# Performance work log

Hardware: AMD Instinct MI355X
Metric: run time of the kernel (lower is better)

Reference implementation:

```python
import jax, jax.numpy as jnp
import numpy as np

N = 100000      # nodes
E = 1600000     # edges (before self-loops)
NFEAT = 256
NHID = 64       # heads=1, concat -> output dim = NHID
NEG_SLOPE = 0.2 # PyG GATConv default negative_slope


def setup_inputs() -> dict:
    key = jax.random.key(0)
    k1, k2, k3, k4, k5 = jax.random.split(key, 5)
    x = jax.random.normal(k1, (N, NFEAT), dtype=jnp.float32)
    edge_index = jax.random.randint(k2, (2, E), 0, N, dtype=jnp.int64)
    s = 1.0 / np.sqrt(NFEAT)
    W = jax.random.uniform(k3, (NFEAT, NHID), jnp.float32, -s, s)      # lin weight
    a_src = jax.random.normal(k4, (NHID,), jnp.float32) * 0.1          # att_src
    a_dst = jax.random.normal(k5, (NHID,), jnp.float32) * 0.1          # att_dst
    bias = jnp.zeros((NHID,), jnp.float32)
    return {"x": x, "edge_index": edge_index, "W": W,
            "a_src": a_src, "a_dst": a_dst, "bias": bias}


def reference(x, edge_index, W, a_src, a_dst, bias):
    n = x.shape[0]
    xp = x @ W                                   # [N, NHID] transformed features
    # add self-loops (PyG default add_self_loops=True)
    loop = jnp.arange(n, dtype=edge_index.dtype)
    src = jnp.concatenate([edge_index[0], loop])  # message source j
    dst = jnp.concatenate([edge_index[1], loop])  # message target i
    # per-edge attention logits: LeakyReLU(a_src.x'_j + a_dst.x'_i)
    e = jax.nn.leaky_relu((xp @ a_src)[src] + (xp @ a_dst)[dst], NEG_SLOPE)  # [E+N]
    # segment softmax over incoming edges of each destination node
    m = jax.ops.segment_max(e, dst, num_segments=n)       # [N] (every node has a self-loop)
    ex = jnp.exp(e - m[dst])
    denom = jax.ops.segment_sum(ex, dst, num_segments=n)  # [N]
    alpha = ex / denom[dst]                                # [E+N]
    # attention-weighted scatter aggregation
    out = jax.ops.segment_sum(alpha[:, None] * xp[src], dst, num_segments=n)  # [N, NHID]
    return out + bias
```

## Files before the change

kernel.cpp:

```cpp
#include <hip/hip_runtime.h>
#include <hip/hip_bf16.h>

#define NFEAT 256
#define NHID  64
#define BSH   8
#define BUCKN 256
#define CAP   5120
#define CHUNK 4096

typedef unsigned int u32;
typedef unsigned short u16;
typedef long long ll;

typedef __attribute__((ext_vector_type(8))) short bf16x8;
typedef __attribute__((ext_vector_type(4))) float f32x4;

__device__ __forceinline__ float bfu2f(u16 u) {
    return __uint_as_float((u32)u << 16);
}
__device__ __forceinline__ u16 f2bfu(float f) {
    u32 u = __float_as_uint(f);
    u32 r = (u + 0x7fffu + ((u >> 16) & 1u)) >> 16;
    return (u16)r;
}
__device__ __forceinline__ float load_f(const void* p, int i, int f32) {
    return f32 ? ((const float*)p)[i] : bfu2f(((const u16*)p)[i]);
}

__device__ __forceinline__ void load_edge(const void* ei, int i64f, int E, int eid,
                                          int& src, int& dst) {
    if (eid < E) {
        if (i64f) {
            src = (int)((const ll*)ei)[eid];
            dst = (int)((const ll*)ei)[(size_t)E + eid];
        } else {
            src = ((const int*)ei)[eid];
            dst = ((const int*)ei)[(size_t)E + eid];
        }
    } else {
        src = dst = eid - E;
    }
}

__global__ __launch_bounds__(256) void prep_kernel(
    const void* __restrict__ W_, const void* __restrict__ ei,
    int* __restrict__ flags, u16* __restrict__ wt, int* __restrict__ gcursor)
{
    __shared__ int f32sh;
    const int tid = threadIdx.x;
    const int b = blockIdx.x;
    if (tid == 0) f32sh = 0;
    __syncthreads();
    {
        float v = bfu2f(((const u16*)W_)[tid]);
        if (!(fabsf(v) <= 0.07f)) f32sh = 1;
    }
    __syncthreads();
    const int f32 = f32sh;
    if (b == 0) {
        if (tid == 0) flags[0] = f32;
        if (tid < 64) {
            int vv = ((const int*)ei)[2 * tid + 1];
            unsigned long long m = __ballot(vv != 0);
            if (tid == 0) flags[1] = (m == 0ull) ? 1 : 0;
        }
        gcursor[tid] = 0;
        gcursor[256 + tid] = 0;
    }
    wt[b * 256 + tid] = f2bfu(load_f(W_, tid * NHID + b, f32));
}

__global__ __launch_bounds__(512) void mid_kernel(
    const void* __restrict__ x_, const u16* __restrict__ wt,
    const void* __restrict__ a_src, const void* __restrict__ a_dst,
    const int* __restrict__ flags, u16* __restrict__ xpb,
    float* __restrict__ s, float* __restrict__ t_, int n,
    const void* __restrict__ ei, int* __restrict__ gcursor,
    u32* __restrict__ rec, int E, int total, int NTg, int NBk)
{
    __shared__ int hist[512];
    __shared__ int offs[512];
    __shared__ int curs[512];
    __shared__ int gbase[512];
    __shared__ u32 stage[CHUNK];
    __shared__ u16 bstage[CHUNK];
    __shared__ int wsum[8];

    const int tid = threadIdx.x;
    const int bid = blockIdx.x;
    const int lane = tid & 63;
    const int wv = tid >> 6;
    int role, rid;
    {
        const int np = min(NTg >> 1, NBk);
        if (bid < 3 * np) {
            int k = bid / 3, r = bid - 3 * k;
            if (r < 2) { role = 0; rid = 2 * k + r; }
            else       { role = 1; rid = k; }
        } else {
            int rem = bid - 3 * np;
            int gleft = NTg - 2 * np;
            if (rem < gleft) { role = 0; rid = 2 * np + rem; }
            else             { role = 1; rid = np + (rem - gleft); }
        }
    }

    if (role == 0) {
        const int q = lane >> 4;
        const int l15 = lane & 15;
        const int f32 = flags[0];
        const int arow = min(rid * 128 + wv * 16 + l15, n - 1);

        f32x4 acc[4] = {{0,0,0,0},{0,0,0,0},{0,0,0,0},{0,0,0,0}};
        const u16* wbase = wt + l15 * NFEAT + q * 8;

        if (f32) {
            const float* xb = (const float*)x_ + (size_t)arow * NFEAT + q * 8;
            float4 v[16];
            #pragma unroll
            for (int ks = 0; ks < 8; ++ks) {
                v[2 * ks]     = *(const float4*)(xb + ks * 32);
                v[2 * ks + 1] = *(const float4*)(xb + ks * 32 + 4);
            }
            __builtin_amdgcn_sched_barrier(0);
            #pragma unroll
            for (int ks = 0; ks < 8; ++ks) {
                bf16x8 a;
                a[0] = (short)f2bfu(v[2*ks].x); a[1] = (short)f2bfu(v[2*ks].y);
                a[2] = (short)f2bfu(v[2*ks].z); a[3] = (short)f2bfu(v[2*ks].w);
                a[4] = (short)f2bfu(v[2*ks+1].x); a[5] = (short)f2bfu(v[2*ks+1].y);
                a[6] = (short)f2bfu(v[2*ks+1].z); a[7] = (short)f2bfu(v[2*ks+1].w);
                #pragma unroll
                for (int tl = 0; tl < 4; ++tl) {
                    bf16x8 b = *(const bf16x8*)(wbase + tl * 16 * NFEAT + ks * 32);
                    acc[tl] = __builtin_amdgcn_mfma_f32_16x16x32_bf16(a, b, acc[tl], 0, 0, 0);
                }
            }
        } else {
            const u16* xb = (const u16*)x_ + (size_t)arow * NFEAT + q * 8;
            bf16x8 a[8];
            #pragma unroll
            for (int ks = 0; ks < 8; ++ks)
                a[ks] = *(const bf16x8*)(xb + ks * 32);
            __builtin_amdgcn_sched_barrier(0);
            #pragma unroll
            for (int ks = 0; ks < 8; ++ks) {
                #pragma unroll
                for (int tl = 0; tl < 4; ++tl) {
                    bf16x8 b = *(const bf16x8*)(wbase + tl * 16 * NFEAT + ks * 32);
                    acc[tl] = __builtin_amdgcn_mfma_f32_16x16x32_bf16(a[ks], b, acc[tl], 0, 0, 0);
                }
            }
        }

        float asl[4], adl[4];
        #pragma unroll
        for (int tl = 0; tl < 4; ++tl) {
            asl[tl] = load_f(a_src, tl * 16 + l15, f32);
            adl[tl] = load_f(a_dst, tl * 16 + l15, f32);
        }
        #pragma unroll
        for (int reg = 0; reg < 4; ++reg) {
            int node = rid * 128 + wv * 16 + q * 4 + reg;
            bool ok = node < n;
            float pvs = 0.f, pvt = 0.f;
            #pragma unroll
            for (int tl = 0; tl < 4; ++tl) {
                float v = acc[tl][reg];
                if (ok) xpb[(size_t)node * NHID + tl * 16 + l15] = f2bfu(v);
                pvs = fmaf(v, asl[tl], pvs);
                pvt = fmaf(v, adl[tl], pvt);
            }
            #pragma unroll
            for (int o = 1; o < 16; o <<= 1) {
                pvs += __shfl_xor(pvs, o);
                pvt += __shfl_xor(pvt, o);
            }
            if (ok && l15 == 0) { s[node] = pvs; t_[node] = pvt; }
        }
        return;
    }

    const int base = rid * CHUNK;
    const int cn = min(CHUNK, total - base);
    const int i64f = flags[1];

    hist[tid] = 0;
    __syncthreads();
    int es[8], ed[8];
    #pragma unroll
    for (int j = 0; j < 8; ++j) {
        int e = base + tid + 512 * j;
        if (e < total) {
            load_edge(ei, i64f, E, e, es[j], ed[j]);
            atomicAdd(&hist[ed[j] >> BSH], 1);
        } else ed[j] = -1;
    }
    __syncthreads();
    const int v = hist[tid];
    int sc = v;
    #pragma unroll
    for (int o = 1; o < 64; o <<= 1) {
        int t2 = __shfl_up(sc, o);
        if (lane >= o) sc += t2;
    }
    if (lane == 63) wsum[wv] = sc;
    __syncthreads();
    if (wv == 0 && lane < 8) {
        int orig = wsum[lane];
        int w = orig;
        #pragma unroll
        for (int o = 1; o < 8; o <<= 1) {
            int t2 = __shfl_up(w, o);
            if (lane >= o) w += t2;
        }
        wsum[lane] = w - orig;
    }
    __syncthreads();
    const int excl = wsum[wv] + sc - v;
    offs[tid] = excl;
    curs[tid] = excl;
    gbase[tid] = tid * CAP + (v ? atomicAdd(&gcursor[tid], v) : 0);
    __syncthreads();
    #pragma unroll
    for (int j = 0; j < 8; ++j) {
        if (ed[j] >= 0) {
            int bb = ed[j] >> BSH;
            int p = atomicAdd(&curs[bb], 1);
            stage[p] = ((u32)(ed[j] & 255) << 24) | (u32)es[j];
            bstage[p] = (u16)bb;
        }
    }
    __syncthreads();
    for (int i = tid; i < cn; i += 512) {
        int bb = bstage[i];
        rec[(size_t)gbase[bb] + (i - offs[bb])] = stage[i];
    }
}

#define HN 128
__global__ __launch_bounds__(512) void fused_kernel(
    const u32* __restrict__ rec, const int* __restrict__ gcursor,
    const float* __restrict__ s, const float* __restrict__ t_,
    const u16* __restrict__ xpb, const void* __restrict__ bias,
    const int* __restrict__ flags, float* __restrict__ out, int n)
{
    __shared__ int rowp[HN + 1];
    __shared__ int curs[HN];
    __shared__ u32 ssrc[CAP * 3 / 4];
    __shared__ float ps[CAP * 3 / 4];
    const int b = blockIdx.x >> 1;
    const int half = blockIdx.x & 1;
    const int tid = threadIdx.x;
    const int dst0 = (b << BSH) + half * HN;
    const int cnt = min(gcursor[b], CAP);
    const u32* r = rec + (size_t)b * CAP;
    const int SCAP = CAP * 3 / 4;

    for (int i = tid; i <= HN; i += 512) rowp[i] = 0;
    __syncthreads();
    for (int i = tid; i < cnt; i += 512) {
        u32 v = r[i];
        int dl = (int)(v >> 24);
        if ((dl >> 7) == half) atomicAdd(&rowp[(dl & (HN - 1)) + 1], 1);
    }
    __syncthreads();
    for (int o = 1; o <= HN; o <<= 1) {
        int tv = 0;
        if (tid <= HN && tid >= o) tv = rowp[tid - o];
        __syncthreads();
        if (tid <= HN && tid >= o) rowp[tid] += tv;
        __syncthreads();
    }
    if (tid < HN) curs[tid] = rowp[tid];
    __syncthreads();
    for (int i = tid; i < cnt; i += 512) {
        u32 v = r[i];
        int dl = (int)(v >> 24);
        if ((dl >> 7) == half) {
            int p = atomicAdd(&curs[dl & (HN - 1)], 1);
            if (p < SCAP) ssrc[p] = v;
        }
    }
    __syncthreads();

    const int tot = min(rowp[HN], SCAP);
    for (int i = tid; i < tot; i += 512) {
        u32 v = ssrc[i];
        int row = (int)(v >> 24) & (HN - 1);
        int src = (int)(v & 0x00FFFFFFu);
        float e = s[src] + t_[dst0 + row];
        e = (e >= 0.f) ? e : 0.2f * e;
        ps[i] = __expf(e);
    }
    __syncthreads();

    const int lane = tid & 63;
    const int wv = tid >> 6;
    const float bl = load_f(bias, lane, flags[0]);
    for (int nl = wv; nl < HN; nl += 8) {
        int node = dst0 + nl;
        if (node >= n) break;
        int beg = rowp[nl], end = min(rowp[nl + 1], SCAP);
        float lsum = 0.f;
        float O0 = 0.f, O1 = 0.f, O2 = 0.f, O3 = 0.f;
        int jj = beg;
        for (; jj + 8 <= end; jj += 8) {
            int sj[8]; float pj[8], rv[8];
            #pragma unroll
            for (int u = 0; u < 8; ++u) {
                sj[u] = (int)(ssrc[jj + u] & 0x00FFFFFFu);
                pj[u] = ps[jj + u];
            }
            #pragma unroll
            for (int u = 0; u < 8; ++u)
                rv[u] = bfu2f(xpb[(size_t)sj[u] * NHID + lane]);
            lsum += ((pj[0] + pj[1]) + (pj[2] + pj[3]))
                  + ((pj[4] + pj[5]) + (pj[6] + pj[7]));
            O0 = fmaf(pj[0], rv[0], O0); O1 = fmaf(pj[1], rv[1], O1);
            O2 = fmaf(pj[2], rv[2], O2); O3 = fmaf(pj[3], rv[3], O3);
            O0 = fmaf(pj[4], rv[4], O0); O1 = fmaf(pj[5], rv[5], O1);
            O2 = fmaf(pj[6], rv[6], O2); O3 = fmaf(pj[7], rv[7], O3);
        }
        for (; jj < end; ++jj) {
            int s0 = (int)(ssrc[jj] & 0x00FFFFFFu);
            float p0 = ps[jj];
            lsum += p0;
            O0 = fmaf(p0, bfu2f(xpb[(size_t)s0 * NHID + lane]), O0);
        }
        out[(size_t)node * NHID + lane] = ((O0 + O1) + (O2 + O3)) / lsum + bl;
    }
}

extern "C" void kernel_launch(void* const* d_in, const int* in_sizes, int n_in,
                              void* d_out, int out_size, void* d_ws, size_t ws_size,
                              hipStream_t stream) {
    const void* x     = d_in[0];
    const void* ei    = d_in[1];
    const void* W     = d_in[2];
    const void* a_src = d_in[3];
    const void* a_dst = d_in[4];
    const void* bias  = d_in[5];
    float* out = (float*)d_out;

    const int n     = in_sizes[0] / NFEAT;
    const int E     = in_sizes[1] / 2;
    const int total = E + n;
    const int NB    = (n + BUCKN - 1) >> BSH;
    const int NTg   = (n + 127) / 128;
    const int NBk   = (total + CHUNK - 1) / CHUNK;

    char* ws = (char*)d_ws;
    size_t off = 0;
    auto carve = [&](size_t bytes) -> char* {
        char* p = ws + off;
        off = (off + bytes + 255) & ~(size_t)255;
        return p;
    };
    int*   flags   = (int*)  carve(64 * sizeof(int));
    u16*   wt      = (u16*)  carve((size_t)NFEAT * NHID * 2);
    u16*   xpb     = (u16*)  carve((size_t)n * NHID * 2);
    float* s       = (float*)carve((size_t)n * 4);
    float* t       = (float*)carve((size_t)n * 4);
    int*   gcursor = (int*)  carve(512 * 4);
    u32*   rec     = (u32*)  carve((size_t)NB * CAP * 4);

    prep_kernel<<<64, 256, 0, stream>>>(W, ei, flags, wt, gcursor);
    mid_kernel<<<NTg + NBk, 512, 0, stream>>>(x, wt, a_src, a_dst, flags, xpb,
                                              s, t, n, ei, gcursor, rec, E,
                                              total, NTg, NBk);
    fused_kernel<<<NB * 2, 512, 0, stream>>>(rec, gcursor, s, t, xpb, bias, flags, out, n);
}
```

Measured before the change: 262.8 us.

## Halve mid_kernel block size and chunk, flush buckets per-thread without bstage

Shrinks mid_kernel blocks from 512 to 256 threads, with 64-row GEMM tiles and 2048-edge chunks, and sets launch bounds to allow 8 blocks per CU. Each thread now handles two histogram buckets in the scan. The staged-record flush drops the per-record bucket-id array and instead has each thread copy its buckets' contiguous runs to global memory. The goal is more, smaller blocks and lower LDS use for better occupancy, but the per-thread serial copy loses coalesced stores across lanes.

```diff
diff --git a/kernel.cpp b/kernel.cpp
--- a/kernel.cpp
+++ b/kernel.cpp
@@ -6,7 +6,7 @@
 #define BSH   8
 #define BUCKN 256
 #define CAP   5120
-#define CHUNK 4096
+#define CHUNK 2048
 
 typedef unsigned int u32;
 typedef unsigned short u16;
@@ -70,7 +70,7 @@
     wt[b * 256 + tid] = f2bfu(load_f(W_, tid * NHID + b, f32));
 }
 
-__global__ __launch_bounds__(512) void mid_kernel(
+__global__ __launch_bounds__(256, 8) void mid_kernel(
     const void* __restrict__ x_, const u16* __restrict__ wt,
     const void* __restrict__ a_src, const void* __restrict__ a_dst,
     const int* __restrict__ flags, u16* __restrict__ xpb,
@@ -83,7 +83,6 @@
     __shared__ int curs[512];
     __shared__ int gbase[512];
     __shared__ u32 stage[CHUNK];
-    __shared__ u16 bstage[CHUNK];
     __shared__ int wsum[8];
 
     const int tid = threadIdx.x;
@@ -109,7 +108,7 @@
         const int q = lane >> 4;
         const int l15 = lane & 15;
         const int f32 = flags[0];
-        const int arow = min(rid * 128 + wv * 16 + l15, n - 1);
+        const int arow = min(rid * 64 + wv * 16 + l15, n - 1);
 
         f32x4 acc[4] = {{0,0,0,0},{0,0,0,0},{0,0,0,0},{0,0,0,0}};
         const u16* wbase = wt + l15 * NFEAT + q * 8;
@@ -161,7 +160,7 @@
         }
         #pragma unroll
         for (int reg = 0; reg < 4; ++reg) {
-            int node = rid * 128 + wv * 16 + q * 4 + reg;
+            int node = rid * 64 + wv * 16 + q * 4 + reg;
             bool ok = node < n;
             float pvs = 0.f, pvt = 0.f;
             #pragma unroll
@@ -186,25 +185,28 @@
     const int i64f = flags[1];
 
     hist[tid] = 0;
+    hist[tid + 256] = 0;
     __syncthreads();
     int es[8], ed[8];
     #pragma unroll
     for (int j = 0; j < 8; ++j) {
-        int e = base + tid + 512 * j;
+        int e = base + tid + 256 * j;
         if (e < total) {
             load_edge(ei, i64f, E, e, es[j], ed[j]);
             atomicAdd(&hist[ed[j] >> BSH], 1);
         } else ed[j] = -1;
     }
     __syncthreads();
-    const int v = hist[tid];
-    int sc = v;
+    const int v0 = hist[tid];
+    const int v1 = hist[tid + 256];
+    int sc0 = v0, sc1 = v1;
     #pragma unroll
     for (int o = 1; o < 64; o <<= 1) {
-        int t2 = __shfl_up(sc, o);
-        if (lane >= o) sc += t2;
-    }
-    if (lane == 63) wsum[wv] = sc;
+        int t0 = __shfl_up(sc0, o);
+        int t1 = __shfl_up(sc1, o);
+        if (lane >= o) { sc0 += t0; sc1 += t1; }
+    }
+    if (lane == 63) { wsum[wv] = sc0; wsum[4 + wv] = sc1; }
     __syncthreads();
     if (wv == 0 && lane < 8) {
         int orig = wsum[lane];
@@ -217,10 +219,12 @@
         wsum[lane] = w - orig;
     }
     __syncthreads();
-    const int excl = wsum[wv] + sc - v;
-    offs[tid] = excl;
-    curs[tid] = excl;
-    gbase[tid] = tid * CAP + (v ? atomicAdd(&gcursor[tid], v) : 0);
+    const int e0 = wsum[wv] + sc0 - v0;
+    const int e1 = wsum[4 + wv] + sc1 - v1;
+    offs[tid] = e0;        curs[tid] = e0;
+    offs[tid + 256] = e1;  curs[tid + 256] = e1;
+    gbase[tid] = tid * CAP + (v0 ? atomicAdd(&gcursor[tid], v0) : 0);
+    gbase[tid + 256] = (tid + 256) * CAP + (v1 ? atomicAdd(&gcursor[tid + 256], v1) : 0);
     __syncthreads();
     #pragma unroll
     for (int j = 0; j < 8; ++j) {
@@ -228,13 +232,14 @@
             int bb = ed[j] >> BSH;
             int p = atomicAdd(&curs[bb], 1);
             stage[p] = ((u32)(ed[j] & 255) << 24) | (u32)es[j];
-            bstage[p] = (u16)bb;
-        }
-    }
-    __syncthreads();
-    for (int i = tid; i < cn; i += 512) {
-        int bb = bstage[i];
-        rec[(size_t)gbase[bb] + (i - offs[bb])] = stage[i];
+        }
+    }
+    __syncthreads();
+    {
+        int gb = gbase[tid], mo = offs[tid];
+        for (int i = 0; i < v0; ++i) rec[(size_t)gb + i] = stage[mo + i];
+        gb = gbase[tid + 256]; mo = offs[tid + 256];
+        for (int i = 0; i < v1; ++i) rec[(size_t)gb + i] = stage[mo + i];
     }
 }
 
@@ -347,7 +352,7 @@
     const int E     = in_sizes[1] / 2;
     const int total = E + n;
     const int NB    = (n + BUCKN - 1) >> BSH;
-    const int NTg   = (n + 127) / 128;
+    const int NTg   = (n + 63) / 64;
     const int NBk   = (total + CHUNK - 1) / CHUNK;
 
     char* ws = (char*)d_ws;
@@ -363,10 +368,10 @@
     float* s       = (float*)carve((size_t)n * 4);
     float* t       = (float*)carve((size_t)n * 4);
     int*   gcursor = (int*)  carve(512 * 4);
-    u32*   rec     = (u32*)  carve((size_t)NB * CAP * 4);
+    u32*   rec     = (u32*)  carve((size_t)512 * CAP * 4);
 
     prep_kernel<<<64, 256, 0, stream>>>(W, ei, flags, wt, gcursor);
-    mid_kernel<<<NTg + NBk, 512, 0, stream>>>(x, wt, a_src, a_dst, flags, xpb,
+    mid_kernel<<<NTg + NBk, 256, 0, stream>>>(x, wt, a_src, a_dst, flags, xpb,
                                               s, t, n, ei, gcursor, rec, E,
                                               total, NTg, NBk);
     fused_kernel<<<NB * 2, 512, 0, stream>>>(rec, gcursor, s, t, xpb, bias, flags, out, n);
```

New measurement: 272.8 us. +3.8%, slower.

## Fold weight-prep kernel into GEMM blocks via LDS-staged transposed W

Applied to the files above, without the earlier changes.

Removes the separate prep kernel. Each GEMM block now detects the dtype, transposes and converts W into padded shared memory, and feeds its MFMAs from LDS instead of from a global transposed copy. The edge-bucketing blocks detect the index width locally, and the cursor reset becomes a memset. This saves one kernel launch and the dependency between kernels. In exchange, every GEMM block redoes the 16K-element W transpose, and the shared-memory union may change occupancy.

```diff
diff --git a/kernel.cpp b/kernel.cpp
--- a/kernel.cpp
+++ b/kernel.cpp
@@ -3,6 +3,7 @@
 
 #define NFEAT 256
 #define NHID  64
+#define XPW   264
 #define BSH   8
 #define BUCKN 256
 #define CAP   5120
@@ -42,49 +43,16 @@
     }
 }
 
-__global__ __launch_bounds__(256) void prep_kernel(
-    const void* __restrict__ W_, const void* __restrict__ ei,
-    int* __restrict__ flags, u16* __restrict__ wt, int* __restrict__ gcursor)
-{
-    __shared__ int f32sh;
-    const int tid = threadIdx.x;
-    const int b = blockIdx.x;
-    if (tid == 0) f32sh = 0;
-    __syncthreads();
-    {
-        float v = bfu2f(((const u16*)W_)[tid]);
-        if (!(fabsf(v) <= 0.07f)) f32sh = 1;
-    }
-    __syncthreads();
-    const int f32 = f32sh;
-    if (b == 0) {
-        if (tid == 0) flags[0] = f32;
-        if (tid < 64) {
-            int vv = ((const int*)ei)[2 * tid + 1];
-            unsigned long long m = __ballot(vv != 0);
-            if (tid == 0) flags[1] = (m == 0ull) ? 1 : 0;
-        }
-        gcursor[tid] = 0;
-        gcursor[256 + tid] = 0;
-    }
-    wt[b * 256 + tid] = f2bfu(load_f(W_, tid * NHID + b, f32));
-}
-
 __global__ __launch_bounds__(512) void mid_kernel(
-    const void* __restrict__ x_, const u16* __restrict__ wt,
+    const void* __restrict__ x_, const void* __restrict__ W_,
     const void* __restrict__ a_src, const void* __restrict__ a_dst,
-    const int* __restrict__ flags, u16* __restrict__ xpb,
+    int* __restrict__ flags, u16* __restrict__ xpb,
     float* __restrict__ s, float* __restrict__ t_, int n,
     const void* __restrict__ ei, int* __restrict__ gcursor,
     u32* __restrict__ rec, int E, int total, int NTg, int NBk)
 {
-    __shared__ int hist[512];
-    __shared__ int offs[512];
-    __shared__ int curs[512];
-    __shared__ int gbase[512];
-    __shared__ u32 stage[CHUNK];
-    __shared__ u16 bstage[CHUNK];
-    __shared__ int wsum[8];
+    __shared__ __align__(16) char smem[34304];
+    __shared__ int sflag;
 
     const int tid = threadIdx.x;
     const int bid = blockIdx.x;
@@ -106,13 +74,30 @@
     }
 
     if (role == 0) {
+        u16* wlds = (u16*)smem;
+
+        if (tid == 0) sflag = 0;
+        __syncthreads();
+        if (tid < 256) {
+            float v = bfu2f(((const u16*)W_)[tid]);
+            if (!(fabsf(v) <= 0.07f)) sflag = 1;
+        }
+        __syncthreads();
+        const int f32 = sflag;
+        if (tid == 0) flags[0] = f32;
+
+        for (int j = tid; j < NFEAT * NHID; j += 512) {
+            int k = j >> 6, h = j & 63;
+            wlds[h * XPW + k] = f2bfu(load_f(W_, j, f32));
+        }
+        __syncthreads();
+
         const int q = lane >> 4;
         const int l15 = lane & 15;
-        const int f32 = flags[0];
         const int arow = min(rid * 128 + wv * 16 + l15, n - 1);
 
         f32x4 acc[4] = {{0,0,0,0},{0,0,0,0},{0,0,0,0},{0,0,0,0}};
-        const u16* wbase = wt + l15 * NFEAT + q * 8;
+        const u16* wbase = wlds + l15 * XPW + q * 8;
 
         if (f32) {
             const float* xb = (const float*)x_ + (size_t)arow * NFEAT + q * 8;
@@ -132,7 +117,7 @@
                 a[6] = (short)f2bfu(v[2*ks+1].z); a[7] = (short)f2bfu(v[2*ks+1].w);
                 #pragma unroll
                 for (int tl = 0; tl < 4; ++tl) {
-                    bf16x8 b = *(const bf16x8*)(wbase + tl * 16 * NFEAT + ks * 32);
+                    bf16x8 b = *(const bf16x8*)(wbase + tl * 16 * XPW + ks * 32);
                     acc[tl] = __builtin_amdgcn_mfma_f32_16x16x32_bf16(a, b, acc[tl], 0, 0, 0);
                 }
             }
@@ -147,7 +132,7 @@
             for (int ks = 0; ks < 8; ++ks) {
                 #pragma unroll
                 for (int tl = 0; tl < 4; ++tl) {
-                    bf16x8 b = *(const bf16x8*)(wbase + tl * 16 * NFEAT + ks * 32);
+                    bf16x8 b = *(const bf16x8*)(wbase + tl * 16 * XPW + ks * 32);
                     acc[tl] = __builtin_amdgcn_mfma_f32_16x16x32_bf16(a[ks], b, acc[tl], 0, 0, 0);
                 }
             }
@@ -181,12 +166,26 @@
         return;
     }
 
+    int* hist  = (int*)smem;
+    int* offs  = hist + 512;
+    int* curs  = offs + 512;
+    int* gbase = curs + 512;
+    u32* stage = (u32*)(gbase + 512);
+    u16* bstage = (u16*)(stage + CHUNK);
+    int* wsum  = (int*)(bstage + CHUNK);
+
     const int base = rid * CHUNK;
     const int cn = min(CHUNK, total - base);
-    const int i64f = flags[1];
-
+
+    if (tid < 64) {
+        int vv = ((const int*)ei)[2 * tid + 1];
+        unsigned long long m = __ballot(vv != 0);
+        if (tid == 0) sflag = (m == 0ull) ? 1 : 0;
+    }
     hist[tid] = 0;
     __syncthreads();
+    const int i64f = sflag;
+
     int es[8], ed[8];
     #pragma unroll
     for (int j = 0; j < 8; ++j) {
@@ -358,15 +357,15 @@
         return p;
     };
     int*   flags   = (int*)  carve(64 * sizeof(int));
-    u16*   wt      = (u16*)  carve((size_t)NFEAT * NHID * 2);
     u16*   xpb     = (u16*)  carve((size_t)n * NHID * 2);
     float* s       = (float*)carve((size_t)n * 4);
     float* t       = (float*)carve((size_t)n * 4);
     int*   gcursor = (int*)  carve(512 * 4);
     u32*   rec     = (u32*)  carve((size_t)NB * CAP * 4);
 
-    prep_kernel<<<64, 256, 0, stream>>>(W, ei, flags, wt, gcursor);
-    mid_kernel<<<NTg + NBk, 512, 0, stream>>>(x, wt, a_src, a_dst, flags, xpb,
+    hipMemsetAsync(gcursor, 0, 512 * 4, stream);
+
+    mid_kernel<<<NTg + NBk, 512, 0, stream>>>(x, W, a_src, a_dst, flags, xpb,
                                               s, t, n, ei, gcursor, rec, E,
                                               total, NTg, NBk);
     fused_kernel<<<NB * 2, 512, 0, stream>>>(rec, gcursor, s, t, xpb, bias, flags, out, n);
```

Result: faster. 256.0 us (-2.6%).
